# Performance work log

Measured on AMD Instinct MI355X. Metric: run time of the kernel, lower is better.

Reference implementation:

```python
import jax, jax.numpy as jnp
import numpy as np

B, N, E = 128, 196, 2048   # batch, num_features (14x14), encoder_dim
D, A = 512, 512            # decoder_dim, attention_dim


def setup_inputs() -> dict:
    key = jax.random.key(0)
    ks = jax.random.split(key, 8)
    s_e = 1.0 / np.sqrt(E)
    s_d = 1.0 / np.sqrt(D)
    s_a = 1.0 / np.sqrt(A)
    return {
        "encoder_out": jax.random.normal(ks[0], (B, N, E), dtype=jnp.float32),
        "decoder_hidden": jax.random.normal(ks[1], (B, D), dtype=jnp.float32),
        "We": jax.random.uniform(ks[2], (E, A), jnp.float32, -s_e, s_e),
        "be": jax.random.uniform(ks[3], (A,), jnp.float32, -s_e, s_e),
        "Wd": jax.random.uniform(ks[4], (D, A), jnp.float32, -s_d, s_d),
        "bd": jax.random.uniform(ks[5], (A,), jnp.float32, -s_d, s_d),
        "Wf": jax.random.uniform(ks[6], (A, 1), jnp.float32, -s_a, s_a),
        "bf": jax.random.uniform(ks[7], (1,), jnp.float32, -s_a, s_a),
    }


def reference(encoder_out, decoder_hidden, We, be, Wd, bd, Wf, bf):
    # att1: [B,N,A] projection of encoder features
    att1 = jnp.einsum('bne,ea->bna', encoder_out, We) + be
    # att2: [B,A] projection of decoder state, broadcast over N
    att2 = decoder_hidden @ Wd + bd
    att = jnp.tanh(att1 + att2[:, None, :])          # [B,N,A]
    scores = jnp.einsum('bna,ao->bno', att, Wf) + bf  # [B,N,1]
    alpha = jax.nn.softmax(scores, axis=1)            # softmax over num_features
    context = jnp.sum(encoder_out * alpha, axis=1)    # [B,E]
    return (context, alpha)
```

## Files before the change

### kernel.cpp

```cpp
#include <hip/hip_runtime.h>
#include <hip/hip_bf16.h>
#include <stdint.h>

#define B_   128
#define N_   196
#define E_   2048
#define D_   512
#define A_   512
#define MTOT (B_ * N_)

typedef short  short8  __attribute__((ext_vector_type(8)));
typedef float  floatx4 __attribute__((ext_vector_type(4)));

__device__ __forceinline__ unsigned short f2bf(float f) {
    union { float f; uint32_t u; } v; v.f = f;
    uint32_t r = v.u + 0x7FFFu + ((v.u >> 16) & 1u);
    return (unsigned short)(r >> 16);
}

__device__ __forceinline__ uint32_t pkbf(float a, float b) {
    uint32_t ua = __float_as_uint(a) + 0x8000u;
    uint32_t ub = __float_as_uint(b) + 0x8000u;
    return __builtin_amdgcn_perm(ub, ua, 0x07060302u);
}

__global__ void transcvt_k(const float* __restrict__ We, unsigned short* __restrict__ WeT) {
    __shared__ float tile[32][33];
    const int e0 = blockIdx.x * 32, a0 = blockIdx.y * 32;
    const int t = threadIdx.x, tc = t & 31, tr = t >> 5;
#pragma unroll
    for (int i = 0; i < 4; ++i) {
        int r = tr + i * 8;
        tile[r][tc] = We[(size_t)(e0 + r) * A_ + a0 + tc];
    }
    __syncthreads();
#pragma unroll
    for (int i = 0; i < 4; ++i) {
        int r = tr + i * 8;
        WeT[(size_t)(a0 + r) * E_ + e0 + tc] = f2bf(tile[tc][r]);
    }
}

__launch_bounds__(512)
__global__ void att2_k(const float* __restrict__ dh, const float* __restrict__ Wd,
                       const float* __restrict__ bd, const float* __restrict__ be,
                       float* __restrict__ att2p) {
    const int b = blockIdx.x, t = threadIdx.x;
    __shared__ float sdh[D_];
    sdh[t] = dh[b * D_ + t];
    __syncthreads();
    float acc = 0.f;
#pragma unroll 8
    for (int d = 0; d < D_; ++d) acc += sdh[d] * Wd[(size_t)d * A_ + t];
    att2p[(size_t)b * A_ + t] = acc + bd[t] + be[t];
}

__launch_bounds__(512, 4)
__global__ void score_gemm(const float* __restrict__ enc,
                           const unsigned short* __restrict__ WeT,
                           const float* __restrict__ att2p,
                           const float* __restrict__ Wf,
                           float* __restrict__ scoresP) {
    __shared__ __align__(16) char sMem[2 * 36864];
    __shared__ float sPart[8][64];

    const int t   = threadIdx.x;
    const int w   = t >> 6;
    const int l   = t & 63;
    const int l15 = l & 15;
    const int q4  = l >> 4;
    const int row0 = blockIdx.x * 64;

    floatx4 acc[4][4] = {};

    const int ar = t >> 3, ap = t & 7;
    const float* aSrcT = enc + (size_t)(row0 + ar) * E_ + ap * 4;
    const int aWr = ar * 64 + (((ap >> 1) ^ ((ar >> 1) & 3)) * 16) + (ap & 1) * 8;

    const unsigned short* bSrc[4];
    int bDst[4];
#pragma unroll
    for (int j = 0; j < 4; ++j) {
        int s = (w * 4 + j) * 64 + l;
        int n = s >> 2, p = s & 3;
        int q = p ^ ((n >> 1) & 3);
        bSrc[j] = WeT + (size_t)n * E_ + q * 8;
        bDst[j] = 4096 + (w * 4 + j) * 1024;
    }

    const int chA  = q4 ^ ((l15 >> 1) & 3);
    const int offA = l15 * 64 + chA * 16;
    const int offB = 4096 + (w * 64 + l15) * 64 + chA * 16;

    {
        float4 a0 = *(const float4*)(aSrcT);
#pragma unroll
        for (int j = 0; j < 4; ++j)
            __builtin_amdgcn_global_load_lds(
                (const __attribute__((address_space(1))) uint32_t*)(bSrc[j]),
                (__attribute__((address_space(3))) uint32_t*)(sMem + bDst[j]), 16, 0, 0);
        uint2 aw;
        aw.x = pkbf(a0.x, a0.y);
        aw.y = pkbf(a0.z, a0.w);
        *(uint2*)(sMem + aWr) = aw;
        __syncthreads();
    }

    int cur = 0;
#pragma unroll 2
    for (int kk = 0; kk < 64; ++kk) {
        const int nxt = cur ^ 36864;
        const int kn  = (kk + 1) & 63;

        float4 aNext = *(const float4*)(aSrcT + kn * 32);
#pragma unroll
        for (int j = 0; j < 4; ++j)
            __builtin_amdgcn_global_load_lds(
                (const __attribute__((address_space(1))) uint32_t*)(bSrc[j] + kn * 32),
                (__attribute__((address_space(3))) uint32_t*)(sMem + nxt + bDst[j]), 16, 0, 0);

        short8 bfr[4];
#pragma unroll
        for (int ni = 0; ni < 4; ++ni)
            bfr[ni] = *(const short8*)(sMem + cur + offB + ni * 1024);
#pragma unroll
        for (int mi = 0; mi < 4; ++mi) {
            short8 a = *(const short8*)(sMem + cur + offA + mi * 1024);
            acc[mi][0] = __builtin_amdgcn_mfma_f32_16x16x32_bf16(a, bfr[0], acc[mi][0], 0, 0, 0);
            acc[mi][1] = __builtin_amdgcn_mfma_f32_16x16x32_bf16(a, bfr[1], acc[mi][1], 0, 0, 0);
            acc[mi][2] = __builtin_amdgcn_mfma_f32_16x16x32_bf16(a, bfr[2], acc[mi][2], 0, 0, 0);
            acc[mi][3] = __builtin_amdgcn_mfma_f32_16x16x32_bf16(a, bfr[3], acc[mi][3], 0, 0, 0);
        }

        uint2 aw;
        aw.x = pkbf(aNext.x, aNext.y);
        aw.y = pkbf(aNext.z, aNext.w);
        *(uint2*)(sMem + nxt + aWr) = aw;
        __syncthreads();
        cur = nxt;
    }

    const int cbase = w * 64;
    float wfv[4];
#pragma unroll
    for (int ni = 0; ni < 4; ++ni) wfv[ni] = Wf[cbase + ni * 16 + l15];

#pragma unroll
    for (int mi = 0; mi < 4; ++mi) {
#pragma unroll
        for (int r = 0; r < 4; ++r) {
            const int m    = mi * 16 + q4 * 4 + r;
            const int grow = row0 + m;
            const int bb   = grow / N_;
            const float* a2 = att2p + (size_t)bb * A_ + cbase;
            float s = 0.f;
#pragma unroll
            for (int ni = 0; ni < 4; ++ni) {
                float v  = acc[mi][ni][r] + a2[ni * 16 + l15];
                float e  = __expf(2.f * v);
                float th = 1.f - 2.f / (e + 1.f);
                s += th * wfv[ni];
            }
            s += __shfl_xor(s, 1);
            s += __shfl_xor(s, 2);
            s += __shfl_xor(s, 4);
            s += __shfl_xor(s, 8);
            if (l15 == 0) sPart[w][m] = s;
        }
    }
    __syncthreads();
    if (t < 64) {
        float v = 0.f;
#pragma unroll
        for (int ww = 0; ww < 8; ++ww) v += sPart[ww][t];
        scoresP[row0 + t] = v;
    }
}

__global__ void softmax_k(const float* __restrict__ sp, float* __restrict__ alpha) {
    const int b = blockIdx.x, t = threadIdx.x;
    const int w = t >> 6, l = t & 63;
    __shared__ float red[8];
    float v = -3.0e38f;
    if (t < N_) v = sp[b * N_ + t];
    float m = v;
#pragma unroll
    for (int off = 32; off >= 1; off >>= 1) m = fmaxf(m, __shfl_xor(m, off));
    if (l == 0) red[w] = m;
    __syncthreads();
    m = fmaxf(fmaxf(red[0], red[1]), fmaxf(red[2], red[3]));
    float e = 0.f;
    if (t < N_) e = __expf(v - m);
    float s = e;
#pragma unroll
    for (int off = 32; off >= 1; off >>= 1) s += __shfl_xor(s, off);
    if (l == 0) red[4 + w] = s;
    __syncthreads();
    s = red[4] + red[5] + red[6] + red[7];
    if (t < N_) alpha[b * N_ + t] = e / s;
}

__launch_bounds__(256)
__global__ void context_k(const float* __restrict__ enc, const float* __restrict__ alpha,
                          float* __restrict__ ctx) {
    const int chunk = blockIdx.x, b = blockIdx.y;
    const int t = threadIdx.x, tn = t >> 6, tc = t & 63;
    __shared__ float  sAl[N_];
    __shared__ float4 sRed[256];
    if (t < N_) sAl[t] = alpha[b * N_ + t];
    __syncthreads();
    const float* base = enc + (size_t)b * N_ * E_ + chunk * 256 + tc * 4;
    float4 a = make_float4(0.f, 0.f, 0.f, 0.f);
#pragma unroll 7
    for (int n = tn; n < N_; n += 4) {
        float  al = sAl[n];
        float4 v  = *(const float4*)(base + (size_t)n * E_);
        a.x += al * v.x; a.y += al * v.y; a.z += al * v.z; a.w += al * v.w;
    }
    sRed[t] = a;
    __syncthreads();
    if (t < 64) {
        float4 r0 = sRed[t], r1 = sRed[t + 64], r2 = sRed[t + 128], r3 = sRed[t + 192];
        float4 o = make_float4(r0.x + r1.x + r2.x + r3.x, r0.y + r1.y + r2.y + r3.y,
                               r0.z + r1.z + r2.z + r3.z, r0.w + r1.w + r2.w + r3.w);
        *(float4*)(ctx + (size_t)b * E_ + chunk * 256 + t * 4) = o;
    }
}

extern "C" void kernel_launch(void* const* d_in, const int* in_sizes, int n_in,
                              void* d_out, int out_size, void* d_ws, size_t ws_size,
                              hipStream_t stream) {
    const float* enc = (const float*)d_in[0];
    const float* dh  = (const float*)d_in[1];
    const float* We  = (const float*)d_in[2];
    const float* be  = (const float*)d_in[3];
    const float* Wd  = (const float*)d_in[4];
    const float* bd  = (const float*)d_in[5];
    const float* Wf  = (const float*)d_in[6];

    float* out   = (float*)d_out;
    float* ctx   = out;
    float* alpha = out + B_ * E_;

    char* ws = (char*)d_ws;
    unsigned short* WeT  = (unsigned short*)ws;
    float* att2p         = (float*)(ws + (2u << 20));
    float* scoresP       = (float*)(ws + (2u << 20) + (256u << 10));

    transcvt_k <<<dim3(E_ / 32, A_ / 32), 256, 0, stream>>>(We, WeT);
    att2_k     <<<dim3(B_),              512, 0, stream>>>(dh, Wd, bd, be, att2p);
    score_gemm <<<dim3(MTOT / 64),       512, 0, stream>>>(enc, WeT, att2p, Wf, scoresP);
    softmax_k  <<<dim3(B_),              256, 0, stream>>>(scoresP, alpha);
    context_k  <<<dim3(E_ / 256, B_),    256, 0, stream>>>(enc, alpha, ctx);
}
```

Measured before the change: 420.1 us.

## Split score GEMM columns across two blocks and fuse softmax into context

The score GEMM now uses 64x256 tiles instead of 64x512. Two blocks per row tile each write partial scores to separate buffers, which doubles the grid and cuts LDS and accumulator registers so occupancy can be higher (launch bound raised to 6). The softmax kernel is merged into the context kernel. Each context block sums the two partial scores and recomputes the softmax for its batch row, and chunk 0 writes alpha. In exchange, the encoder A tile is read and converted twice, and the softmax is computed redundantly across chunks.

Measured after the change: 479.8 us. 1.14x slower.

```diff
diff --git a/kernel.cpp b/kernel.cpp
--- a/kernel.cpp
+++ b/kernel.cpp
@@ -55,13 +55,13 @@
     att2p[(size_t)b * A_ + t] = acc + bd[t] + be[t];
 }
 
-__launch_bounds__(512, 4)
+__launch_bounds__(512, 6)
 __global__ void score_gemm(const float* __restrict__ enc,
                            const unsigned short* __restrict__ WeT,
                            const float* __restrict__ att2p,
                            const float* __restrict__ Wf,
                            float* __restrict__ scoresP) {
-    __shared__ __align__(16) char sMem[2 * 36864];
+    __shared__ __align__(16) char sMem[2 * 20480];
     __shared__ float sPart[8][64];
 
     const int t   = threadIdx.x;
@@ -69,33 +69,36 @@
     const int l   = t & 63;
     const int l15 = l & 15;
     const int q4  = l >> 4;
-    const int row0 = blockIdx.x * 64;
-
-    floatx4 acc[4][4] = {};
+    const int rowBlk = blockIdx.x >> 1;
+    const int half   = blockIdx.x & 1;
+    const int row0   = rowBlk * 64;
+    const int col0   = half * 256;
+
+    floatx4 acc[4][2] = {};
 
     const int ar = t >> 3, ap = t & 7;
     const float* aSrcT = enc + (size_t)(row0 + ar) * E_ + ap * 4;
     const int aWr = ar * 64 + (((ap >> 1) ^ ((ar >> 1) & 3)) * 16) + (ap & 1) * 8;
 
-    const unsigned short* bSrc[4];
-    int bDst[4];
-#pragma unroll
-    for (int j = 0; j < 4; ++j) {
-        int s = (w * 4 + j) * 64 + l;
-        int n = s >> 2, p = s & 3;
+    const unsigned short* bSrc[2];
+    int bDst[2];
+#pragma unroll
+    for (int j = 0; j < 2; ++j) {
+        int s = w * 2 + j;
+        int n = s * 16 + (l >> 2), p = l & 3;
         int q = p ^ ((n >> 1) & 3);
-        bSrc[j] = WeT + (size_t)n * E_ + q * 8;
-        bDst[j] = 4096 + (w * 4 + j) * 1024;
+        bSrc[j] = WeT + (size_t)(col0 + n) * E_ + q * 8;
+        bDst[j] = 4096 + s * 1024;
     }
 
     const int chA  = q4 ^ ((l15 >> 1) & 3);
     const int offA = l15 * 64 + chA * 16;
-    const int offB = 4096 + (w * 64 + l15) * 64 + chA * 16;
+    const int offB = 4096 + (w * 32 + l15) * 64 + chA * 16;
 
     {
         float4 a0 = *(const float4*)(aSrcT);
 #pragma unroll
-        for (int j = 0; j < 4; ++j)
+        for (int j = 0; j < 2; ++j)
             __builtin_amdgcn_global_load_lds(
                 (const __attribute__((address_space(1))) uint32_t*)(bSrc[j]),
                 (__attribute__((address_space(3))) uint32_t*)(sMem + bDst[j]), 16, 0, 0);
@@ -109,27 +112,25 @@
     int cur = 0;
 #pragma unroll 2
     for (int kk = 0; kk < 64; ++kk) {
-        const int nxt = cur ^ 36864;
+        const int nxt = cur ^ 20480;
         const int kn  = (kk + 1) & 63;
 
         float4 aNext = *(const float4*)(aSrcT + kn * 32);
 #pragma unroll
-        for (int j = 0; j < 4; ++j)
+        for (int j = 0; j < 2; ++j)
             __builtin_amdgcn_global_load_lds(
                 (const __attribute__((address_space(1))) uint32_t*)(bSrc[j] + kn * 32),
                 (__attribute__((address_space(3))) uint32_t*)(sMem + nxt + bDst[j]), 16, 0, 0);
 
-        short8 bfr[4];
-#pragma unroll
-        for (int ni = 0; ni < 4; ++ni)
+        short8 bfr[2];
+#pragma unroll
+        for (int ni = 0; ni < 2; ++ni)
             bfr[ni] = *(const short8*)(sMem + cur + offB + ni * 1024);
 #pragma unroll
         for (int mi = 0; mi < 4; ++mi) {
             short8 a = *(const short8*)(sMem + cur + offA + mi * 1024);
             acc[mi][0] = __builtin_amdgcn_mfma_f32_16x16x32_bf16(a, bfr[0], acc[mi][0], 0, 0, 0);
             acc[mi][1] = __builtin_amdgcn_mfma_f32_16x16x32_bf16(a, bfr[1], acc[mi][1], 0, 0, 0);
-            acc[mi][2] = __builtin_amdgcn_mfma_f32_16x16x32_bf16(a, bfr[2], acc[mi][2], 0, 0, 0);
-            acc[mi][3] = __builtin_amdgcn_mfma_f32_16x16x32_bf16(a, bfr[3], acc[mi][3], 0, 0, 0);
         }
 
         uint2 aw;
@@ -140,10 +141,10 @@
         cur = nxt;
     }
 
-    const int cbase = w * 64;
-    float wfv[4];
-#pragma unroll
-    for (int ni = 0; ni < 4; ++ni) wfv[ni] = Wf[cbase + ni * 16 + l15];
+    const int cbase = col0 + w * 32;
+    float wfv[2];
+#pragma unroll
+    for (int ni = 0; ni < 2; ++ni) wfv[ni] = Wf[cbase + ni * 16 + l15];
 
 #pragma unroll
     for (int mi = 0; mi < 4; ++mi) {
@@ -155,7 +156,7 @@
             const float* a2 = att2p + (size_t)bb * A_ + cbase;
             float s = 0.f;
 #pragma unroll
-            for (int ni = 0; ni < 4; ++ni) {
+            for (int ni = 0; ni < 2; ++ni) {
                 float v  = acc[mi][ni][r] + a2[ni * 16 + l15];
                 float e  = __expf(2.f * v);
                 float th = 1.f - 2.f / (e + 1.f);
@@ -173,16 +174,22 @@
         float v = 0.f;
 #pragma unroll
         for (int ww = 0; ww < 8; ++ww) v += sPart[ww][t];
-        scoresP[row0 + t] = v;
-    }
-}
-
-__global__ void softmax_k(const float* __restrict__ sp, float* __restrict__ alpha) {
-    const int b = blockIdx.x, t = threadIdx.x;
-    const int w = t >> 6, l = t & 63;
-    __shared__ float red[8];
+        scoresP[(size_t)half * MTOT + row0 + t] = v;
+    }
+}
+
+__launch_bounds__(256)
+__global__ void ctx_sm_k(const float* __restrict__ enc, const float* __restrict__ sp,
+                         float* __restrict__ alpha, float* __restrict__ ctx) {
+    const int chunk = blockIdx.x, b = blockIdx.y;
+    const int t = threadIdx.x, w = t >> 6, l = t & 63;
+    const int tn = t >> 6, tc = t & 63;
+    __shared__ float  sAl[N_];
+    __shared__ float  red[8];
+    __shared__ float4 sRed[256];
+
     float v = -3.0e38f;
-    if (t < N_) v = sp[b * N_ + t];
+    if (t < N_) v = sp[b * N_ + t] + sp[MTOT + b * N_ + t];
     float m = v;
 #pragma unroll
     for (int off = 32; off >= 1; off >>= 1) m = fmaxf(m, __shfl_xor(m, off));
@@ -197,25 +204,20 @@
     if (l == 0) red[4 + w] = s;
     __syncthreads();
     s = red[4] + red[5] + red[6] + red[7];
-    if (t < N_) alpha[b * N_ + t] = e / s;
-}
-
-__launch_bounds__(256)
-__global__ void context_k(const float* __restrict__ enc, const float* __restrict__ alpha,
-                          float* __restrict__ ctx) {
-    const int chunk = blockIdx.x, b = blockIdx.y;
-    const int t = threadIdx.x, tn = t >> 6, tc = t & 63;
-    __shared__ float  sAl[N_];
-    __shared__ float4 sRed[256];
-    if (t < N_) sAl[t] = alpha[b * N_ + t];
-    __syncthreads();
+    if (t < N_) {
+        float al = e / s;
+        sAl[t] = al;
+        if (chunk == 0) alpha[b * N_ + t] = al;
+    }
+    __syncthreads();
+
     const float* base = enc + (size_t)b * N_ * E_ + chunk * 256 + tc * 4;
     float4 a = make_float4(0.f, 0.f, 0.f, 0.f);
 #pragma unroll 7
     for (int n = tn; n < N_; n += 4) {
         float  al = sAl[n];
-        float4 v  = *(const float4*)(base + (size_t)n * E_);
-        a.x += al * v.x; a.y += al * v.y; a.z += al * v.z; a.w += al * v.w;
+        float4 vv = *(const float4*)(base + (size_t)n * E_);
+        a.x += al * vv.x; a.y += al * vv.y; a.z += al * vv.z; a.w += al * vv.w;
     }
     sRed[t] = a;
     __syncthreads();
@@ -249,7 +251,6 @@
 
     transcvt_k <<<dim3(E_ / 32, A_ / 32), 256, 0, stream>>>(We, WeT);
     att2_k     <<<dim3(B_),              512, 0, stream>>>(dh, Wd, bd, be, att2p);
-    score_gemm <<<dim3(MTOT / 64),       512, 0, stream>>>(enc, WeT, att2p, Wf, scoresP);
-    softmax_k  <<<dim3(B_),              256, 0, stream>>>(scoresP, alpha);
-    context_k  <<<dim3(E_ / 256, B_),    256, 0, stream>>>(enc, alpha, ctx);
-}
+    score_gemm <<<dim3(2 * MTOT / 64),   512, 0, stream>>>(enc, WeT, att2p, Wf, scoresP);
+    ctx_sm_k   <<<dim3(E_ / 256, B_),    256, 0, stream>>>(enc, scoresP, alpha, ctx);
+}
```
